# Kernel optimization log

Hardware: AMD Instinct MI355X
Metric: run time of the kernel (lower is better)

## Reference

```python
import jax, jax.numpy as jnp
import numpy as np

B, N, DIM, HEADS, DIM_HEAD = 2, 2048, 1024, 16, 64
SCALE = DIM_HEAD ** -0.5


def setup_inputs() -> dict:
    key = jax.random.key(0)
    k1, k2, k3, k4, k5 = jax.random.split(key, 5)
    x = jax.random.normal(k1, (B, N, DIM), dtype=jnp.float32)
    causal_boundary_indices = jax.random.randint(k2, (B,), 0, N)
    # Parameters
    Wq = jax.random.normal(k3, (HEADS, DIM, DIM_HEAD), dtype=jnp.float32) * (DIM ** -0.5)
    Wkv = jax.random.normal(k4, (DIM, 2 * DIM_HEAD), dtype=jnp.float32) * (DIM ** -0.5)
    Wo = jax.random.normal(k5, (HEADS * DIM_HEAD, DIM), dtype=jnp.float32) * ((HEADS * DIM_HEAD) ** -0.5)
    return {"x": x, "Wq": Wq, "Wkv": Wkv, "Wo": Wo,
            "causal_boundary_indices": causal_boundary_indices}


def reference(x, Wq, Wkv, Wo, causal_boundary_indices):
    b, n, d = x.shape
    # Multi-query attention: per-head Q, single shared K/V head
    q = jnp.einsum('bnd,hde->bhne', x, Wq) * SCALE          # [b,h,n,dh]
    kv = x @ Wkv                                            # [b,n,2*dh]
    k, v = jnp.split(kv, 2, axis=-1)                        # [b,n,dh] each
    sim = jnp.einsum('bhid,bjd->bhij', q, k)                # [b,h,n,n]
    max_neg = -jnp.finfo(sim.dtype).max
    seq = jnp.arange(n)
    causal_mask = seq[None, :] > seq[:, None]               # [n,n] True = masked
    # positions j < boundary[b] are fully visible (prefix-LM); only j >= boundary obey causality
    mask_after = seq[None, None, None, :] >= causal_boundary_indices[:, None, None, None]
    mask = causal_mask[None, None, :, :] & mask_after       # [b,1,n,n]
    sim = jnp.where(mask, max_neg, sim)
    attn = jax.nn.softmax(sim, axis=-1)
    out = jnp.einsum('bhij,bjd->bhid', attn, v)             # [b,h,n,dh]
    out = out.transpose(0, 2, 1, 3).reshape(b, n, -1)       # [b,n,h*dh]
    return out @ Wo                                         # [b,n,d]
```

## Files before the change

kernel.cpp:

```cpp
#include <hip/hip_runtime.h>
#include <hip/hip_bf16.h>

typedef unsigned short ushort_t;
typedef unsigned int u32;
typedef __attribute__((ext_vector_type(8))) short bf16x8;
typedef __attribute__((ext_vector_type(4))) float f32x4;
typedef __attribute__((ext_vector_type(16))) float f32x16;
typedef __attribute__((ext_vector_type(2))) unsigned int u32x2;

#define L2E 1.44269504f

__device__ __forceinline__ ushort_t f2bf(float f) {
    union { __hip_bfloat16 b; ushort_t u; } c;
    c.b = __float2bfloat16(f);
    return c.u;
}

__device__ __forceinline__ f32x4 mfma16(bf16x8 a, bf16x8 b, f32x4 c) {
    return __builtin_amdgcn_mfma_f32_16x16x32_bf16(a, b, c, 0, 0, 0);
}

__device__ __forceinline__ f32x16 mfma32(bf16x8 a, bf16x8 b, f32x16 c) {
    return __builtin_amdgcn_mfma_f32_32x32x16_bf16(a, b, c, 0, 0, 0);
}

__device__ __forceinline__ u32 cvtpk(float lo, float hi) {
    u32 r;
    asm("v_cvt_pk_bf16_f32 %0, %1, %2" : "=v"(r) : "v"(lo), "v"(hi));
    return r;
}

__device__ __forceinline__ u32x2 pl32swap(u32 a, u32 b) {
#if __has_builtin(__builtin_amdgcn_permlane32_swap)
    auto r = __builtin_amdgcn_permlane32_swap((int)a, (int)b, false, false);
    return u32x2{(u32)r[0], (u32)r[1]};
#else
    u32 sa = (u32)__shfl_xor((int)a, 32);
    u32 sb = (u32)__shfl_xor((int)b, 32);
    int lane = threadIdx.x & 63;
    u32 d = (lane >= 32) ? sb : a;
    u32 s = (lane >= 32) ? b : sa;
    return u32x2{d, s};
#endif
}

__device__ __forceinline__ float swap32f(float x, int hi) {
    union { float f; u32 u; } c; c.f = x;
    u32x2 r = pl32swap(c.u, c.u);
    union { u32 u; float f; } o; o.u = hi ? r[0] : r[1];
    return o.f;
}

__device__ __forceinline__ void gload_lds16(const ushort_t* g, ushort_t* l) {
    __builtin_amdgcn_global_load_lds(
        (const __attribute__((address_space(1))) unsigned int*)g,
        (__attribute__((address_space(3))) unsigned int*)l, 16, 0, 0);
}


__device__ __forceinline__ int perm_off(int row, int k) {
    return (((row >> 6) & 1) * 8 + ((row >> 4) & 3) * 2 + ((k >> 5) & 1)) * 512
         + (row & 15) * 8 + ((k >> 3) & 3) * 128 + (k & 7);
}

__global__ __launch_bounds__(256)
void convert_kernel(const float* __restrict__ x, const float* __restrict__ Wq,
                    const float* __restrict__ Wkv, const float* __restrict__ Wo,
                    ushort_t* __restrict__ Xp, ushort_t* __restrict__ W1p,
                    ushort_t* __restrict__ Wop) {
    int idx = blockIdx.x * 256 + threadIdx.x;
    if (idx < 524288) {
        int row = idx >> 7, k = (idx & 127) << 3;
        const float* src = x + (size_t)row * 1024 + k;
        f32x4 a = *(const f32x4*)src, c2 = *(const f32x4*)(src + 4);
        union { u32 u[4]; bf16x8 v; } P;
        P.u[0] = cvtpk(a[0], a[1]);  P.u[1] = cvtpk(a[2], a[3]);
        P.u[2] = cvtpk(c2[0], c2[1]); P.u[3] = cvtpk(c2[2], c2[3]);
        size_t tile = (size_t)((row >> 7) * 16 + (k >> 6));
        *(bf16x8*)(Xp + tile * 8192 + perm_off(row, k)) = P.v;
        return;
    }
    idx -= 524288;
    if (idx < 147456) {
        int c = idx >> 7, k = (idx & 127) << 3;
        float v[8];
        if (c < 1024) {
            const float* s = Wq + ((size_t)(c >> 6) * 1024 + k) * 64 + (c & 63);
#pragma unroll
            for (int e = 0; e < 8; e++) v[e] = s[(size_t)e * 64] * 0.125f;
        } else {
            const float* s = Wkv + (size_t)k * 128 + (c - 1024);
#pragma unroll
            for (int e = 0; e < 8; e++) v[e] = s[(size_t)e * 128];
        }
        union { u32 u[4]; bf16x8 vv; } P;
        P.u[0] = cvtpk(v[0], v[1]); P.u[1] = cvtpk(v[2], v[3]);
        P.u[2] = cvtpk(v[4], v[5]); P.u[3] = cvtpk(v[6], v[7]);
        size_t tile = (size_t)((c >> 7) * 16 + (k >> 6));
        *(bf16x8*)(W1p + tile * 8192 + perm_off(c, k)) = P.vv;
        return;
    }
    idx -= 147456;
    if (idx < 131072) {
        int j = idx >> 7, k = (idx & 127) << 3;
        const float* s = Wo + (size_t)k * 1024 + j;
        float v[8];
#pragma unroll
        for (int e = 0; e < 8; e++) v[e] = s[(size_t)e * 1024];
        union { u32 u[4]; bf16x8 vv; } P;
        P.u[0] = cvtpk(v[0], v[1]); P.u[1] = cvtpk(v[2], v[3]);
        P.u[2] = cvtpk(v[4], v[5]); P.u[3] = cvtpk(v[6], v[7]);
        size_t tile = (size_t)((j >> 7) * 16 + (k >> 6));
        *(bf16x8*)(Wop + tile * 8192 + perm_off(j, k)) = P.vv;
    }
}

template <int MODE>
__global__ __launch_bounds__(256, 3)
void gemmp(const ushort_t* __restrict__ Ap, const ushort_t* __restrict__ Bp,
           ushort_t* __restrict__ Cq, ushort_t* __restrict__ Ck,
           ushort_t* __restrict__ Cv, float* __restrict__ Cf) {
    __shared__ ushort_t smem[2][12288];
    const int tid = threadIdx.x, lane = tid & 63, w = tid >> 6;
    const int wm = w >> 1, wn = w & 1, l15 = lane & 15, g = lane >> 4;
    const int tm = blockIdx.x, tn = blockIdx.y;
    constexpr int KT = 16;

    f32x4 acc[2][4];
#pragma unroll
    for (int i = 0; i < 2; i++)
#pragma unroll
        for (int j = 0; j < 4; j++) acc[i][j] = (f32x4)(0.f);

    const ushort_t* Atile = Ap + ((size_t)(tm >> 1) * 16) * 8192 + (tm & 1) * 8 * 512;
    const ushort_t* Btile = Bp + ((size_t)tn * 16) * 8192;

    auto stage = [&](int buf, int kt) {
#pragma unroll
        for (int j = 0; j < 6; j++) {
            const int s = w * 6 + j;
            const ushort_t* gp = (s < 8)
                ? Atile + (size_t)kt * 8192 + s * 512 + lane * 8
                : Btile + (size_t)kt * 8192 + (s - 8) * 512 + lane * 8;
            gload_lds16(gp, &smem[buf][s * 512]);
        }
    };

    stage(0, 0);
    asm volatile("s_waitcnt vmcnt(0)" ::: "memory");
    __syncthreads();
    int cur = 0;
    for (int kt = 0; kt < KT; ++kt) {
        if (kt + 1 < KT) stage(cur ^ 1, kt + 1);
#pragma unroll
        for (int kc = 0; kc < 2; kc++) {
            bf16x8 af[2], bfr[4];
#pragma unroll
            for (int mi = 0; mi < 2; mi++)
                af[mi] = *(const bf16x8*)&smem[cur][((wm * 2 + mi) * 2 + kc) * 512 + lane * 8];
#pragma unroll
            for (int ni = 0; ni < 4; ni++)
                bfr[ni] = *(const bf16x8*)&smem[cur][(8 + wn * 8 + ni * 2 + kc) * 512 + lane * 8];
            __builtin_amdgcn_s_setprio(1);
#pragma unroll
            for (int mi = 0; mi < 2; mi++)
#pragma unroll
                for (int ni = 0; ni < 4; ni++)
                    acc[mi][ni] = mfma16(af[mi], bfr[ni], acc[mi][ni]);
            __builtin_amdgcn_s_setprio(0);
        }
        asm volatile("s_waitcnt vmcnt(0)" ::: "memory");
        __syncthreads();
        cur ^= 1;
    }

#pragma unroll
    for (int mi = 0; mi < 2; mi++)
#pragma unroll
        for (int ni = 0; ni < 4; ni++)
#pragma unroll
            for (int r = 0; r < 4; r++) {
                int row = tm * 64 + wm * 32 + mi * 16 + 4 * g + r;
                int col = tn * 128 + wn * 64 + ni * 16 + l15;
                float v = acc[mi][ni][r];
                if (MODE == 0) {
                    if (col < 1024) {
                        Cq[(size_t)row * 1024 + col] = f2bf(v);
                    } else if (col < 1088) {
                        int e = col - 1024;
                        int n = row & 2047, bb = row >> 11;
                        int t = n >> 6;
                        int idx = t * 4096 + (((n >> 5) & 1) * 4 + (e >> 4)) * 512 +
                                  (((e >> 3) & 1) * 32 + (n & 31)) * 8 + (e & 7);
                        Ck[(size_t)bb * 131072 + idx] = f2bf(v);
                    } else {
                        int d = col - 1088;
                        int n = row & 2047, bb = row >> 11;
                        int t = n >> 6;
                        int idx = t * 4096 + ((d >> 5) * 4 + ((n >> 4) & 3)) * 512 +
                                  (((n >> 3) & 1) * 32 + (d & 31)) * 8 + (n & 7);
                        Cv[(size_t)bb * 131072 + idx] = f2bf(v);
                    }
                } else {
                    Cf[(size_t)row * 1024 + col] = v;
                }
            }
}

__global__ __launch_bounds__(256, 2)
void attn32(const ushort_t* __restrict__ Qb, const ushort_t* __restrict__ Kt,
            const ushort_t* __restrict__ Vt2, ushort_t* __restrict__ Ob,
            const int* __restrict__ bnds) {
    __shared__ ushort_t sK[2][4096];
    __shared__ ushort_t sV[2][4096];
    const int tid = threadIdx.x;
    const int lane = tid & 63;
    const int w = tid >> 6;
    const int l31 = lane & 31;
    const int hi = lane >> 5;

    const int id = blockIdx.x;
    const int s = id & 255;
    const int flip = id >> 8;
    const int b = s >> 7;
    const int qt5 = (s >> 2) & 31;
    const int hg = s & 3;
    const int qt = flip ? 63 - qt5 : qt5;
    const int h = hg * 4 + w;
    const int bnd = bnds[b];
    const int qbase = qt * 32;
    const int q = qbase + l31;

    const ushort_t* Qp = Qb + ((size_t)(b * 2048 + q)) * 1024 + h * 64 + hi * 8;
    bf16x8 Qf[4];
#pragma unroll
    for (int kk = 0; kk < 4; kk++) Qf[kk] = *(const bf16x8*)(Qp + kk * 16);

    f32x16 oacc0 = (f32x16)(0.f), oacc1 = (f32x16)(0.f);
    float m = -3e38f, lsum = 0.f;

    int wl = qbase + 31;
    if (bnd - 1 > wl) wl = bnd - 1;
    if (wl > 2047) wl = 2047;
    const int niter = (wl >> 6) + 1;

    const ushort_t* Kglob = Kt + (size_t)b * 131072;
    const ushort_t* Vglob = Vt2 + (size_t)b * 131072;

    auto stage = [&](int buf, int t) {
        if (w < 2) {
            const ushort_t* g = Kglob + (size_t)t * 4096 + (w * 4) * 512 + lane * 8;
            ushort_t* l = &sK[buf][(w * 4) * 512];
#pragma unroll
            for (int j = 0; j < 4; j++) gload_lds16(g + j * 512, l + j * 512);
        } else {
            const ushort_t* g = Vglob + (size_t)t * 4096 + ((w - 2) * 4) * 512 + lane * 8;
            ushort_t* l = &sV[buf][((w - 2) * 4) * 512];
#pragma unroll
            for (int j = 0; j < 4; j++) gload_lds16(g + j * 512, l + j * 512);
        }
    };

    stage(0, 0);
    asm volatile("s_waitcnt vmcnt(0)" ::: "memory");
    __syncthreads();

    int cur = 0;
    for (int it = 0; it < niter; ++it) {
        const int k0 = it * 64;
        if (it + 1 < niter) stage(cur ^ 1, it + 1);

        bf16x8 kfr[8];
#pragma unroll
        for (int r = 0; r < 8; r++)
            kfr[r] = *(const bf16x8*)&sK[cur][r * 512 + lane * 8];
        f32x16 s0 = (f32x16)(0.f), s1 = (f32x16)(0.f);
        __builtin_amdgcn_s_setprio(1);
#pragma unroll
        for (int kk = 0; kk < 4; kk++) {
            s0 = mfma32(kfr[kk], Qf[kk], s0);
            s1 = mfma32(kfr[4 + kk], Qf[kk], s1);
        }
        __builtin_amdgcn_s_setprio(0);

        const bool fullvis = (k0 + 63 <= qbase) || (k0 + 63 < bnd);
        if (!fullvis) {
#pragma unroll
            for (int r = 0; r < 16; r++) {
                int key0 = k0 + (r & 3) + 8 * (r >> 2) + 4 * hi;
                if (key0 > q && key0 >= bnd) s0[r] = -3e38f;
                int key1 = key0 + 32;
                if (key1 > q && key1 >= bnd) s1[r] = -3e38f;
            }
        }

        float tmax = fmaxf(s0[0], s0[1]);
#pragma unroll
        for (int r = 2; r < 16; r++) tmax = fmaxf(tmax, s0[r]);
#pragma unroll
        for (int r = 0; r < 16; r++) tmax = fmaxf(tmax, s1[r]);
        tmax = fmaxf(tmax, swap32f(tmax, hi));

        if (!__all(tmax <= m + 8.0f)) {
            float mnew = fmaxf(m, tmax);
            float alpha = __builtin_amdgcn_exp2f((m - mnew) * L2E);
#pragma unroll
            for (int r = 0; r < 16; r++) { oacc0[r] *= alpha; oacc1[r] *= alpha; }
            lsum *= alpha;
            m = mnew;
        }
        const float mL = m * L2E;

        bf16x8 vfr[8];
#pragma unroll
        for (int r = 0; r < 8; r++)
            vfr[r] = *(const bf16x8*)&sV[cur][r * 512 + lane * 8];

        __builtin_amdgcn_s_setprio(1);
#pragma unroll
        for (int c = 0; c < 4; c++) {
            float p0, p1, p2, p3, p4, p5, p6, p7;
            {
                const f32x16& sc = (c < 2) ? s0 : s1;
                const int base = (c & 1) * 8;
                p0 = __builtin_amdgcn_exp2f(sc[base + 0] * L2E - mL);
                p1 = __builtin_amdgcn_exp2f(sc[base + 1] * L2E - mL);
                p2 = __builtin_amdgcn_exp2f(sc[base + 2] * L2E - mL);
                p3 = __builtin_amdgcn_exp2f(sc[base + 3] * L2E - mL);
                p4 = __builtin_amdgcn_exp2f(sc[base + 4] * L2E - mL);
                p5 = __builtin_amdgcn_exp2f(sc[base + 5] * L2E - mL);
                p6 = __builtin_amdgcn_exp2f(sc[base + 6] * L2E - mL);
                p7 = __builtin_amdgcn_exp2f(sc[base + 7] * L2E - mL);
            }
            lsum += ((p0 + p1) + (p2 + p3)) + ((p4 + p5) + (p6 + p7));
            u32 a0 = cvtpk(p0, p1);
            u32 c0 = cvtpk(p2, p3);
            u32 b0 = cvtpk(p4, p5);
            u32 d0 = cvtpk(p6, p7);
            u32x2 r02 = pl32swap(a0, b0);
            u32x2 r13 = pl32swap(c0, d0);
            union { u32 u[4]; bf16x8 v; } P;
            P.u[0] = r02[0]; P.u[1] = r13[0]; P.u[2] = r02[1]; P.u[3] = r13[1];
            oacc0 = mfma32(vfr[c], P.v, oacc0);
            oacc1 = mfma32(vfr[4 + c], P.v, oacc1);
        }
        __builtin_amdgcn_s_setprio(0);

        asm volatile("s_waitcnt vmcnt(0)" ::: "memory");
        __syncthreads();
        cur ^= 1;
    }

    const float ltot = lsum + swap32f(lsum, hi);
    const float li = 1.f / ltot;

    const int rowO = b * 2048 + q;
    const int segbase = ((rowO >> 6) & 1) * 8 + ((rowO >> 4) & 3) * 2;
    ushort_t* ObT = Ob + ((size_t)(rowO >> 7) * 16 + h) * 8192 + (rowO & 15) * 8 + 4 * hi;
#pragma unroll
    for (int dh = 0; dh < 2; dh++)
#pragma unroll
        for (int rq = 0; rq < 4; rq++) {
            union { ushort_t s[4]; u32x2 u; } st;
#pragma unroll
            for (int j = 0; j < 4; j++) {
                float v = (dh == 0 ? oacc0[4 * rq + j] : oacc1[4 * rq + j]) * li;
                st.s[j] = f2bf(v);
            }
            *(u32x2*)(ObT + (segbase + dh) * 512 + rq * 128) = st.u;
        }
}

extern "C" void kernel_launch(void* const* d_in, const int* in_sizes, int n_in,
                              void* d_out, int out_size, void* d_ws, size_t ws_size,
                              hipStream_t stream) {
    const float* x   = (const float*)d_in[0];
    const float* Wq  = (const float*)d_in[1];
    const float* Wkv = (const float*)d_in[2];
    const float* Wo  = (const float*)d_in[3];
    const int* bnds  = (const int*)d_in[4];
    char* ws = (char*)d_ws;
    ushort_t* Xbf  = (ushort_t*)(ws);
    ushort_t* W1bt = (ushort_t*)(ws + 8388608);
    ushort_t* Wobt = (ushort_t*)(ws + 10747904);
    ushort_t* Qb   = (ushort_t*)(ws + 12845056);
    ushort_t* Kb   = (ushort_t*)(ws + 21233664);
    ushort_t* Vt   = (ushort_t*)(ws + 21757952);
    ushort_t* Ob   = (ushort_t*)(ws + 22282240);
    float* out = (float*)d_out;

    convert_kernel<<<dim3(3136), dim3(256), 0, stream>>>(x, Wq, Wkv, Wo, Xbf, W1bt, Wobt);
    gemmp<0><<<dim3(64, 9), dim3(256), 0, stream>>>(Xbf, W1bt, Qb, Kb, Vt, (float*)nullptr);
    attn32<<<dim3(512), dim3(256), 0, stream>>>(Qb, Kb, Vt, Ob, bnds);
    gemmp<1><<<dim3(64, 8), dim3(256), 0, stream>>>(Ob, Wobt, (ushort_t*)nullptr,
                                                    (ushort_t*)nullptr, (ushort_t*)nullptr, out);
}
```

Before: 97.77 us.

## Split attention KV range across two wave groups and coalesce weight conversion reads

The attention kernel now runs 512 threads per block: two groups of four waves each process alternate 64-key tiles for the same query tile and heads, and their partial softmax states are merged through shared memory at the end. This doubles the waves working on each long causal/prefix row, targeting the latency of the serial KV loop and tail imbalance, at the cost of more shared memory per block and an extra merge step. Separately, the weight conversion now reads fp32 weights with contiguous vector loads and writes scattered 2-byte bf16 stores, replacing strided gathers.

```diff
diff --git a/kernel.cpp b/kernel.cpp
--- a/kernel.cpp
+++ b/kernel.cpp
@@ -81,37 +81,27 @@
         return;
     }
     idx -= 524288;
-    if (idx < 147456) {
-        int c = idx >> 7, k = (idx & 127) << 3;
-        float v[8];
+    if (idx < 294912) {
+        int k = idx / 288, c = (idx % 288) * 4;
+        f32x4 v;
         if (c < 1024) {
-            const float* s = Wq + ((size_t)(c >> 6) * 1024 + k) * 64 + (c & 63);
-#pragma unroll
-            for (int e = 0; e < 8; e++) v[e] = s[(size_t)e * 64] * 0.125f;
+            v = *(const f32x4*)(Wq + ((size_t)((c >> 6) * 1024 + k)) * 64 + (c & 63));
+            v *= 0.125f;
         } else {
-            const float* s = Wkv + (size_t)k * 128 + (c - 1024);
-#pragma unroll
-            for (int e = 0; e < 8; e++) v[e] = s[(size_t)e * 128];
+            v = *(const f32x4*)(Wkv + (size_t)k * 128 + (c - 1024));
         }
-        union { u32 u[4]; bf16x8 vv; } P;
-        P.u[0] = cvtpk(v[0], v[1]); P.u[1] = cvtpk(v[2], v[3]);
-        P.u[2] = cvtpk(v[4], v[5]); P.u[3] = cvtpk(v[6], v[7]);
-        size_t tile = (size_t)((c >> 7) * 16 + (k >> 6));
-        *(bf16x8*)(W1p + tile * 8192 + perm_off(c, k)) = P.vv;
+        ushort_t* base = W1p + (size_t)((c >> 7) * 16 + (k >> 6)) * 8192;
+#pragma unroll
+        for (int i = 0; i < 4; i++) base[perm_off(c + i, k)] = f2bf(v[i]);
         return;
     }
-    idx -= 147456;
-    if (idx < 131072) {
-        int j = idx >> 7, k = (idx & 127) << 3;
-        const float* s = Wo + (size_t)k * 1024 + j;
-        float v[8];
-#pragma unroll
-        for (int e = 0; e < 8; e++) v[e] = s[(size_t)e * 1024];
-        union { u32 u[4]; bf16x8 vv; } P;
-        P.u[0] = cvtpk(v[0], v[1]); P.u[1] = cvtpk(v[2], v[3]);
-        P.u[2] = cvtpk(v[4], v[5]); P.u[3] = cvtpk(v[6], v[7]);
-        size_t tile = (size_t)((j >> 7) * 16 + (k >> 6));
-        *(bf16x8*)(Wop + tile * 8192 + perm_off(j, k)) = P.vv;
+    idx -= 294912;
+    if (idx < 262144) {
+        int k = idx >> 8, j = (idx & 255) * 4;
+        f32x4 v = *(const f32x4*)(Wo + (size_t)k * 1024 + j);
+        ushort_t* base = Wop + (size_t)((j >> 7) * 16 + (k >> 6)) * 8192;
+#pragma unroll
+        for (int i = 0; i < 4; i++) base[perm_off(j + i, k)] = f2bf(v[i]);
     }
 }
 
@@ -207,17 +197,19 @@
             }
 }
 
-__global__ __launch_bounds__(256, 2)
+__global__ __launch_bounds__(512)
+__attribute__((amdgpu_waves_per_eu(4, 4)))
 void attn32(const ushort_t* __restrict__ Qb, const ushort_t* __restrict__ Kt,
             const ushort_t* __restrict__ Vt2, ushort_t* __restrict__ Ob,
             const int* __restrict__ bnds) {
-    __shared__ ushort_t sK[2][4096];
-    __shared__ ushort_t sV[2][4096];
+    __shared__ ushort_t smem[2][16384];
     const int tid = threadIdx.x;
     const int lane = tid & 63;
     const int w = tid >> 6;
     const int l31 = lane & 31;
     const int hi = lane >> 5;
+    const int split = w >> 2;
+    const int hw = w & 3;
 
     const int id = blockIdx.x;
     const int s = id & 255;
@@ -226,7 +218,7 @@
     const int qt5 = (s >> 2) & 31;
     const int hg = s & 3;
     const int qt = flip ? 63 - qt5 : qt5;
-    const int h = hg * 4 + w;
+    const int h = hg * 4 + hw;
     const int bnd = bnds[b];
     const int qbase = qt * 32;
     const int q = qbase + l31;
@@ -243,22 +235,20 @@
     if (bnd - 1 > wl) wl = bnd - 1;
     if (wl > 2047) wl = 2047;
     const int niter = (wl >> 6) + 1;
+    const int nrounds = (niter + 1) >> 1;
 
     const ushort_t* Kglob = Kt + (size_t)b * 131072;
     const ushort_t* Vglob = Vt2 + (size_t)b * 131072;
 
-    auto stage = [&](int buf, int t) {
-        if (w < 2) {
-            const ushort_t* g = Kglob + (size_t)t * 4096 + (w * 4) * 512 + lane * 8;
-            ushort_t* l = &sK[buf][(w * 4) * 512];
-#pragma unroll
-            for (int j = 0; j < 4; j++) gload_lds16(g + j * 512, l + j * 512);
-        } else {
-            const ushort_t* g = Vglob + (size_t)t * 4096 + ((w - 2) * 4) * 512 + lane * 8;
-            ushort_t* l = &sV[buf][((w - 2) * 4) * 512];
-#pragma unroll
-            for (int j = 0; j < 4; j++) gload_lds16(g + j * 512, l + j * 512);
-        }
+    const int stp = w >> 2, skv = (w >> 1) & 1, shf = w & 1;
+    const ushort_t* sgbase = (skv ? Vglob : Kglob) + shf * 2048 + lane * 8;
+    const int sldst = stp * 8192 + skv * 4096 + shf * 2048;
+    auto stage = [&](int buf, int r) {
+        int t = 2 * r + stp;
+        const ushort_t* g = sgbase + (size_t)t * 4096;
+        ushort_t* l = &smem[buf][sldst];
+#pragma unroll
+        for (int j = 0; j < 4; j++) gload_lds16(g + j * 512, l + j * 512);
     };
 
     stage(0, 0);
@@ -266,85 +256,90 @@
     __syncthreads();
 
     int cur = 0;
-    for (int it = 0; it < niter; ++it) {
-        const int k0 = it * 64;
-        if (it + 1 < niter) stage(cur ^ 1, it + 1);
-
-        bf16x8 kfr[8];
-#pragma unroll
-        for (int r = 0; r < 8; r++)
-            kfr[r] = *(const bf16x8*)&sK[cur][r * 512 + lane * 8];
-        f32x16 s0 = (f32x16)(0.f), s1 = (f32x16)(0.f);
-        __builtin_amdgcn_s_setprio(1);
-#pragma unroll
-        for (int kk = 0; kk < 4; kk++) {
-            s0 = mfma32(kfr[kk], Qf[kk], s0);
-            s1 = mfma32(kfr[4 + kk], Qf[kk], s1);
+    for (int r = 0; r < nrounds; ++r) {
+        if (r + 1 < nrounds) stage(cur ^ 1, r + 1);
+        const int t = 2 * r + split;
+        if (t < niter) {
+            const int k0 = t * 64;
+            const ushort_t* kb = &smem[cur][split * 8192];
+            const ushort_t* vb = kb + 4096;
+
+            bf16x8 kfr[8];
+#pragma unroll
+            for (int r8 = 0; r8 < 8; r8++)
+                kfr[r8] = *(const bf16x8*)&kb[r8 * 512 + lane * 8];
+            f32x16 s0 = (f32x16)(0.f), s1 = (f32x16)(0.f);
+            __builtin_amdgcn_s_setprio(1);
+#pragma unroll
+            for (int kk = 0; kk < 4; kk++) {
+                s0 = mfma32(kfr[kk], Qf[kk], s0);
+                s1 = mfma32(kfr[4 + kk], Qf[kk], s1);
+            }
+            __builtin_amdgcn_s_setprio(0);
+
+            const bool fullvis = (k0 + 63 <= qbase) || (k0 + 63 < bnd);
+            if (!fullvis) {
+#pragma unroll
+                for (int rr = 0; rr < 16; rr++) {
+                    int key0 = k0 + (rr & 3) + 8 * (rr >> 2) + 4 * hi;
+                    if (key0 > q && key0 >= bnd) s0[rr] = -3e38f;
+                    int key1 = key0 + 32;
+                    if (key1 > q && key1 >= bnd) s1[rr] = -3e38f;
+                }
+            }
+
+            float tmax = fmaxf(s0[0], s0[1]);
+#pragma unroll
+            for (int rr = 2; rr < 16; rr++) tmax = fmaxf(tmax, s0[rr]);
+#pragma unroll
+            for (int rr = 0; rr < 16; rr++) tmax = fmaxf(tmax, s1[rr]);
+            tmax = fmaxf(tmax, swap32f(tmax, hi));
+
+            if (!__all(tmax <= m + 8.0f)) {
+                float mnew = fmaxf(m, tmax);
+                float alpha = __builtin_amdgcn_exp2f((m - mnew) * L2E);
+#pragma unroll
+                for (int rr = 0; rr < 16; rr++) { oacc0[rr] *= alpha; oacc1[rr] *= alpha; }
+                lsum *= alpha;
+                m = mnew;
+            }
+            const float mL = m * L2E;
+
+            bf16x8 vfr[8];
+#pragma unroll
+            for (int r8 = 0; r8 < 8; r8++)
+                vfr[r8] = *(const bf16x8*)&vb[r8 * 512 + lane * 8];
+
+            __builtin_amdgcn_s_setprio(1);
+#pragma unroll
+            for (int c = 0; c < 4; c++) {
+                float p0, p1, p2, p3, p4, p5, p6, p7;
+                {
+                    const f32x16& sc = (c < 2) ? s0 : s1;
+                    const int base = (c & 1) * 8;
+                    p0 = __builtin_amdgcn_exp2f(sc[base + 0] * L2E - mL);
+                    p1 = __builtin_amdgcn_exp2f(sc[base + 1] * L2E - mL);
+                    p2 = __builtin_amdgcn_exp2f(sc[base + 2] * L2E - mL);
+                    p3 = __builtin_amdgcn_exp2f(sc[base + 3] * L2E - mL);
+                    p4 = __builtin_amdgcn_exp2f(sc[base + 4] * L2E - mL);
+                    p5 = __builtin_amdgcn_exp2f(sc[base + 5] * L2E - mL);
+                    p6 = __builtin_amdgcn_exp2f(sc[base + 6] * L2E - mL);
+                    p7 = __builtin_amdgcn_exp2f(sc[base + 7] * L2E - mL);
+                }
+                lsum += ((p0 + p1) + (p2 + p3)) + ((p4 + p5) + (p6 + p7));
+                u32 a0 = cvtpk(p0, p1);
+                u32 c0 = cvtpk(p2, p3);
+                u32 b0 = cvtpk(p4, p5);
+                u32 d0 = cvtpk(p6, p7);
+                u32x2 r02 = pl32swap(a0, b0);
+                u32x2 r13 = pl32swap(c0, d0);
+                union { u32 u[4]; bf16x8 v; } P;
+                P.u[0] = r02[0]; P.u[1] = r13[0]; P.u[2] = r02[1]; P.u[3] = r13[1];
+                oacc0 = mfma32(vfr[c], P.v, oacc0);
+                oacc1 = mfma32(vfr[4 + c], P.v, oacc1);
+            }
+            __builtin_amdgcn_s_setprio(0);
         }
-        __builtin_amdgcn_s_setprio(0);
-
-        const bool fullvis = (k0 + 63 <= qbase) || (k0 + 63 < bnd);
-        if (!fullvis) {
-#pragma unroll
-            for (int r = 0; r < 16; r++) {
-                int key0 = k0 + (r & 3) + 8 * (r >> 2) + 4 * hi;
-                if (key0 > q && key0 >= bnd) s0[r] = -3e38f;
-                int key1 = key0 + 32;
-                if (key1 > q && key1 >= bnd) s1[r] = -3e38f;
-            }
-        }
-
-        float tmax = fmaxf(s0[0], s0[1]);
-#pragma unroll
-        for (int r = 2; r < 16; r++) tmax = fmaxf(tmax, s0[r]);
-#pragma unroll
-        for (int r = 0; r < 16; r++) tmax = fmaxf(tmax, s1[r]);
-        tmax = fmaxf(tmax, swap32f(tmax, hi));
-
-        if (!__all(tmax <= m + 8.0f)) {
-            float mnew = fmaxf(m, tmax);
-            float alpha = __builtin_amdgcn_exp2f((m - mnew) * L2E);
-#pragma unroll
-            for (int r = 0; r < 16; r++) { oacc0[r] *= alpha; oacc1[r] *= alpha; }
-            lsum *= alpha;
-            m = mnew;
-        }
-        const float mL = m * L2E;
-
-        bf16x8 vfr[8];
-#pragma unroll
-        for (int r = 0; r < 8; r++)
-            vfr[r] = *(const bf16x8*)&sV[cur][r * 512 + lane * 8];
-
-        __builtin_amdgcn_s_setprio(1);
-#pragma unroll
-        for (int c = 0; c < 4; c++) {
-            float p0, p1, p2, p3, p4, p5, p6, p7;
-            {
-                const f32x16& sc = (c < 2) ? s0 : s1;
-                const int base = (c & 1) * 8;
-                p0 = __builtin_amdgcn_exp2f(sc[base + 0] * L2E - mL);
-                p1 = __builtin_amdgcn_exp2f(sc[base + 1] * L2E - mL);
-                p2 = __builtin_amdgcn_exp2f(sc[base + 2] * L2E - mL);
-                p3 = __builtin_amdgcn_exp2f(sc[base + 3] * L2E - mL);
-                p4 = __builtin_amdgcn_exp2f(sc[base + 4] * L2E - mL);
-                p5 = __builtin_amdgcn_exp2f(sc[base + 5] * L2E - mL);
-                p6 = __builtin_amdgcn_exp2f(sc[base + 6] * L2E - mL);
-                p7 = __builtin_amdgcn_exp2f(sc[base + 7] * L2E - mL);
-            }
-            lsum += ((p0 + p1) + (p2 + p3)) + ((p4 + p5) + (p6 + p7));
-            u32 a0 = cvtpk(p0, p1);
-            u32 c0 = cvtpk(p2, p3);
-            u32 b0 = cvtpk(p4, p5);
-            u32 d0 = cvtpk(p6, p7);
-            u32x2 r02 = pl32swap(a0, b0);
-            u32x2 r13 = pl32swap(c0, d0);
-            union { u32 u[4]; bf16x8 v; } P;
-            P.u[0] = r02[0]; P.u[1] = r13[0]; P.u[2] = r02[1]; P.u[3] = r13[1];
-            oacc0 = mfma32(vfr[c], P.v, oacc0);
-            oacc1 = mfma32(vfr[4 + c], P.v, oacc1);
-        }
-        __builtin_amdgcn_s_setprio(0);
 
         asm volatile("s_waitcnt vmcnt(0)" ::: "memory");
         __syncthreads();
@@ -352,23 +347,42 @@
     }
 
     const float ltot = lsum + swap32f(lsum, hi);
-    const float li = 1.f / ltot;
-
-    const int rowO = b * 2048 + q;
-    const int segbase = ((rowO >> 6) & 1) * 8 + ((rowO >> 4) & 3) * 2;
-    ushort_t* ObT = Ob + ((size_t)(rowO >> 7) * 16 + h) * 8192 + (rowO & 15) * 8 + 4 * hi;
-#pragma unroll
-    for (int dh = 0; dh < 2; dh++)
-#pragma unroll
-        for (int rq = 0; rq < 4; rq++) {
-            union { ushort_t s[4]; u32x2 u; } st;
-#pragma unroll
-            for (int j = 0; j < 4; j++) {
-                float v = (dh == 0 ? oacc0[4 * rq + j] : oacc1[4 * rq + j]) * li;
-                st.s[j] = f2bf(v);
-            }
-            *(u32x2*)(ObT + (segbase + dh) * 512 + rq * 128) = st.u;
-        }
+
+    float* mg = (float*)&smem[0][0];
+    if (split == 1) {
+        float* dst = &mg[(hw * 64 + lane) * 34];
+#pragma unroll
+        for (int i = 0; i < 16; i++) { dst[i] = oacc0[i]; dst[16 + i] = oacc1[i]; }
+        dst[32] = m;
+        dst[33] = ltot;
+    }
+    __syncthreads();
+    if (split == 0) {
+        const float* src = &mg[(hw * 64 + lane) * 34];
+        const float mB = src[32], lB = src[33];
+        const float mf = fmaxf(m, mB);
+        const float aA = __builtin_amdgcn_exp2f((m - mf) * L2E);
+        const float aB = __builtin_amdgcn_exp2f((mB - mf) * L2E);
+        const float li = 1.f / (ltot * aA + lB * aB);
+
+        const int rowO = b * 2048 + q;
+        const int segbase = ((rowO >> 6) & 1) * 8 + ((rowO >> 4) & 3) * 2;
+        ushort_t* ObT = Ob + ((size_t)(rowO >> 7) * 16 + h) * 8192 + (rowO & 15) * 8 + 4 * hi;
+#pragma unroll
+        for (int dh = 0; dh < 2; dh++)
+#pragma unroll
+            for (int rq = 0; rq < 4; rq++) {
+                union { ushort_t s[4]; u32x2 u; } st;
+#pragma unroll
+                for (int j = 0; j < 4; j++) {
+                    const int idx = 4 * rq + j;
+                    float a = (dh == 0) ? oacc0[idx] : oacc1[idx];
+                    float v = (a * aA + src[dh * 16 + idx] * aB) * li;
+                    st.s[j] = f2bf(v);
+                }
+                *(u32x2*)(ObT + (segbase + dh) * 512 + rq * 128) = st.u;
+            }
+    }
 }
 
 extern "C" void kernel_launch(void* const* d_in, const int* in_sizes, int n_in,
@@ -389,9 +403,9 @@
     ushort_t* Ob   = (ushort_t*)(ws + 22282240);
     float* out = (float*)d_out;
 
-    convert_kernel<<<dim3(3136), dim3(256), 0, stream>>>(x, Wq, Wkv, Wo, Xbf, W1bt, Wobt);
+    convert_kernel<<<dim3(4224), dim3(256), 0, stream>>>(x, Wq, Wkv, Wo, Xbf, W1bt, Wobt);
     gemmp<0><<<dim3(64, 9), dim3(256), 0, stream>>>(Xbf, W1bt, Qb, Kb, Vt, (float*)nullptr);
-    attn32<<<dim3(512), dim3(256), 0, stream>>>(Qb, Kb, Vt, Ob, bnds);
+    attn32<<<dim3(512), dim3(512), 0, stream>>>(Qb, Kb, Vt, Ob, bnds);
     gemmp<1><<<dim3(64, 8), dim3(256), 0, stream>>>(Ob, Wobt, (ushort_t*)nullptr,
                                                     (ushort_t*)nullptr, (ushort_t*)nullptr, out);
 }
```

Measured after the change: 103.4 us. +5.7%, slower.
